# Optimization experiments

Measured on AMD Instinct MI355X. Metric: run time of the kernel, lower is better.

## Reference

```python
import jax, jax.numpy as jnp
import numpy as np

D = 1024      # input_dim
H = 16        # head_num
HD = 64       # head_dim
HID = 4096    # mlp hidden
CUR = 512     # cur_seq
PREV = 512    # prev_seq (memory)
FULL = CUR + PREV
BS = 16
SCALE = 1.0 / (HD ** 0.5)


def setup_inputs() -> dict:
    key = jax.random.key(0)
    ks = jax.random.split(key, 20)
    def nrm(k, shape, s=0.02):
        return (jax.random.normal(k, shape) * s).astype(jnp.float32)
    inp = {
        "inputs": nrm(ks[0], (CUR, BS, D), 1.0),
        "pos_embedding": nrm(ks[1], (FULL, 1, D), 1.0),
        "u": nrm(ks[2], (H, HD)),
        "v": nrm(ks[3], (H, HD)),
        "memory": nrm(ks[4], (PREV, BS, D), 1.0),
        # causal mask: position i (query) may attend to j <= i + PREV; True = masked
        "mask": jnp.triu(jnp.ones((CUR, FULL), dtype=bool), k=PREV + 1)[:, :, None],
        # attention params (stored as (in, out); torch Linear applies x @ W.T + b)
        "Wkv": nrm(ks[5], (D, 2 * H * HD)), "bkv": jnp.zeros((2 * H * HD,), jnp.float32),
        "Wq": nrm(ks[6], (D, H * HD)), "bq": jnp.zeros((H * HD,), jnp.float32),
        "Wo": nrm(ks[7], (H * HD, D)), "bo": jnp.zeros((D,), jnp.float32),
        "Wp": nrm(ks[8], (D, H * HD)), "bp": jnp.zeros((H * HD,), jnp.float32),
        # layernorms
        "ln1_g": jnp.ones((D,), jnp.float32), "ln1_b": jnp.zeros((D,), jnp.float32),
        "ln2_g": jnp.ones((D,), jnp.float32), "ln2_b": jnp.zeros((D,), jnp.float32),
        # mlp (mlp_num=2): Linear(D,HID)+relu, Linear(HID,D)+relu
        "W1": nrm(ks[9], (D, HID)), "b1": jnp.zeros((HID,), jnp.float32),
        "W2": nrm(ks[10], (HID, D)), "b2": jnp.zeros((D,), jnp.float32),
        # GRU gates: stacked [Wr,Wz,Wg] and [Ur,Uz,Ug], no bias; bg init 2.0
        "g1_W": nrm(ks[11], (3, D, D)), "g1_U": nrm(ks[12], (3, D, D)),
        "g1_bg": jnp.full((D,), 2.0, jnp.float32),
        "g2_W": nrm(ks[13], (3, D, D)), "g2_U": nrm(ks[14], (3, D, D)),
        "g2_bg": jnp.full((D,), 2.0, jnp.float32),
    }
    return inp


def _layernorm(x, g, b, eps=1e-5):
    mu = jnp.mean(x, axis=-1, keepdims=True)
    var = jnp.mean(jnp.square(x - mu), axis=-1, keepdims=True)
    return (x - mu) * jax.lax.rsqrt(var + eps) * g + b


def _rel_shift(x):
    # x: (bs, head, cur, full) -> pad/reshape/slice trick of Transformer-XL
    b, h, c, f = x.shape
    xp = jnp.pad(x, ((0, 0), (0, 0), (0, 0), (1, 0)))      # (b,h,c,f+1)
    xp = xp.reshape(b, h, f + 1, c)
    return xp[:, :, 1:, :].reshape(b, h, c, f)


def _gru_gate(x, y, W, U, bg):
    # W, U: (3, D, D) for [r, z, g] gates; torch Linear => y @ W[i].T
    r = jax.nn.sigmoid(y @ W[0].T + x @ U[0].T)
    z = jax.nn.sigmoid(y @ W[1].T + x @ U[1].T - bg)
    h = jnp.tanh(y @ W[2].T + (r * x) @ U[2].T)
    return (1.0 - z) * x + z * h


def _attention_xl(x_cur, pos_emb, x_full, u, v, mask,
                  Wkv, bkv, Wq, bq, Wo, bo, Wp, bp):
    cur, bs, _ = x_cur.shape
    full = x_full.shape[0]
    kv = x_full @ Wkv + bkv                                  # (full, bs, 2*H*HD)
    key, value = jnp.split(kv, 2, axis=-1)
    query = x_cur @ Wq + bq                                  # (cur, bs, H*HD)
    r = (pos_emb @ Wp + bp).reshape(full, H, HD)             # (full, H, HD)

    key = key.reshape(full, bs, H, HD)
    value = value.reshape(full, bs, H, HD)
    query = query.reshape(cur, bs, H, HD)

    content = jnp.einsum('ibhd,jbhd->bhij', query + u, key)  # (bs,H,cur,full)
    position = jnp.einsum('ibhd,jhd->bhij', query + v, r)    # (bs,H,cur,full)
    position = _rel_shift(position)

    attn = (content + position) * SCALE
    # mask: (cur, full, 1) bool, True = masked
    m = mask[:, :, 0][None, None]                            # (1,1,cur,full)
    attn = jnp.where(m, -jnp.inf, attn)
    p = jax.nn.softmax(attn, axis=-1)

    out = jnp.einsum('bhij,jbhd->ibhd', p, value).reshape(cur, bs, H * HD)
    return out @ Wo + bo                                     # (cur, bs, D)


def reference(inputs, pos_embedding, u, v, memory, mask,
              Wkv, bkv, Wq, bq, Wo, bo, Wp, bp,
              ln1_g, ln1_b, ln2_g, ln2_b,
              W1, b1, W2, b2,
              g1_W, g1_U, g1_bg, g2_W, g2_U, g2_bg):
    prev = memory.shape[0]
    full_input = jnp.concatenate([memory, inputs], axis=0)   # (full, bs, D)
    x1 = _layernorm(full_input, ln1_g, ln1_b)
    a1 = _attention_xl(x1[prev:], pos_embedding, x1, u, v, mask,
                       Wkv, bkv, Wq, bq, Wo, bo, Wp, bp)
    a1 = jax.nn.relu(a1)                                     # dropout = identity (eval)
    o1 = _gru_gate(inputs, a1, g1_W, g1_U, g1_bg)
    x2 = _layernorm(o1, ln2_g, ln2_b)
    m2 = jax.nn.relu(jax.nn.relu(x2 @ W1 + b1) @ W2 + b2)    # mlp: act after every linear
    o2 = _gru_gate(o1, m2, g2_W, g2_U, g2_bg)
    return o2
```

## Files before the change

kernel.cpp:

```cpp
#include <hip/hip_runtime.h>
#include <stdint.h>

typedef _Float16 h16;
typedef __attribute__((ext_vector_type(8))) _Float16 f16x8;
typedef __attribute__((ext_vector_type(4))) _Float16 f16x4;
typedef __attribute__((ext_vector_type(4))) float f32x4;

enum { F_OBF = 1, F_BIAS = 2, F_RELU = 4, F_ACC = 8, F_DUAL = 16 };

#define BARRIER_MEM                                  \
  do {                                               \
    asm volatile("" ::: "memory");                   \
    __builtin_amdgcn_s_barrier();                    \
    asm volatile("" ::: "memory");                   \
  } while (0)

static __device__ __forceinline__ void gload16(const void* g, void* l) {
  __builtin_amdgcn_global_load_lds((__attribute__((address_space(1))) void*)g,
                                   (__attribute__((address_space(3))) void*)l,
                                   16, 0, 0);
}

template <int BN, int FLAGS>
__global__ __launch_bounds__(512) void gemm2_k(
    const h16* __restrict__ A, const h16* __restrict__ B,
    void* __restrict__ Cv, const float* __restrict__ bias,
    int K, int lda, int ldb, int ldc, int gm,
    void* __restrict__ C2v, const float* __restrict__ bias2) {
  constexpr int NH = BN / 128;
  constexpr int WN = BN / 4;
  __shared__ h16 Al[2][256][64];
  __shared__ h16 Bl[2][BN][64];

  const int tid = threadIdx.x, lane = tid & 63, wid = tid >> 6;
  const int wr = wid >> 2, wn = wid & 3;
  const int ar = lane & 15, q4 = lane >> 4;

  const int nwg = gridDim.x, cpx = nwg >> 3;
  const int bid = (blockIdx.x & 7) * cpx + (blockIdx.x >> 3);
  const int mx = bid % gm, ny = bid / gm;

  const h16* Ab = A + (long)mx * 256 * lda;
  const h16* Bb = B + (long)ny * BN * ldb;

  auto stageA = [&](int buf, int half, int k0) {
#pragma unroll
    for (int l = 0; l < 2; ++l) {
      const int idx = l * 512 + tid;
      const int row = half * 128 + (idx >> 3), sl = idx & 7;
      gload16(Ab + (long)row * lda + k0 + (sl ^ (row & 7)) * 8,
              (char*)&Al[buf][0][0] + (half * 1024 + l * 512 + wid * 64) * 16);
    }
  };
  auto stageB = [&](int buf, int half, int k0) {
#pragma unroll
    for (int l = 0; l < NH; ++l) {
      const int idx = l * 512 + tid;
      const int row = half * (BN / 2) + (idx >> 3), sl = idx & 7;
      gload16(Bb + (long)row * ldb + k0 + (sl ^ (row & 7)) * 8,
              (char*)&Bl[buf][0][0] + (half * (BN * 4) + l * 512 + wid * 64) * 16);
    }
  };

  f32x4 acc[8][2 * NH] = {};
  const int nk = K >> 6;

  stageB(0, 0, 0); stageB(0, 1, 0); stageA(0, 0, 0); stageA(0, 1, 0);
  if (nk > 1) { stageB(1, 0, 64); stageB(1, 1, 64); stageA(1, 0, 64); stageA(1, 1, 64); }
  if (nk > 1) {
    if constexpr (NH == 2) asm volatile("s_waitcnt vmcnt(8)" ::: "memory");
    else                   asm volatile("s_waitcnt vmcnt(6)" ::: "memory");
  } else {
    asm volatile("s_waitcnt vmcnt(0)" ::: "memory");
  }
  BARRIER_MEM;

  for (int kt = 0; kt < nk; ++kt) {
    const int b = kt & 1;
    const int k2 = (kt + 2) << 6;
    const bool pf = (kt + 2) < nk;

    f16x8 a0[4][2], b0[NH][2];
#pragma unroll
    for (int m = 0; m < 4; ++m) {
      const int row = wr * 128 + m * 16 + ar;
#pragma unroll
      for (int ks = 0; ks < 2; ++ks)
        a0[m][ks] = *(const f16x8*)&Al[b][row][((ks * 4 + q4) ^ (row & 7)) * 8];
    }
#pragma unroll
    for (int n = 0; n < NH; ++n) {
      const int row = wn * WN + n * 16 + ar;
#pragma unroll
      for (int ks = 0; ks < 2; ++ks)
        b0[n][ks] = *(const f16x8*)&Bl[b][row][((ks * 4 + q4) ^ (row & 7)) * 8];
    }
    BARRIER_MEM;
    __builtin_amdgcn_s_setprio(1);
#pragma unroll
    for (int m = 0; m < 4; ++m)
#pragma unroll
      for (int n = 0; n < NH; ++n)
#pragma unroll
        for (int ks = 0; ks < 2; ++ks)
          acc[m][n] = __builtin_amdgcn_mfma_f32_16x16x32_f16(a0[m][ks], b0[n][ks], acc[m][n], 0, 0, 0);
    __builtin_amdgcn_s_setprio(0);
    BARRIER_MEM;

    f16x8 b1f[NH][2];
#pragma unroll
    for (int n = 0; n < NH; ++n) {
      const int row = wn * WN + (n + NH) * 16 + ar;
#pragma unroll
      for (int ks = 0; ks < 2; ++ks)
        b1f[n][ks] = *(const f16x8*)&Bl[b][row][((ks * 4 + q4) ^ (row & 7)) * 8];
    }
    BARRIER_MEM;
    __builtin_amdgcn_s_setprio(1);
#pragma unroll
    for (int m = 0; m < 4; ++m)
#pragma unroll
      for (int n = 0; n < NH; ++n)
#pragma unroll
        for (int ks = 0; ks < 2; ++ks)
          acc[m][n + NH] = __builtin_amdgcn_mfma_f32_16x16x32_f16(a0[m][ks], b1f[n][ks], acc[m][n + NH], 0, 0, 0);
    __builtin_amdgcn_s_setprio(0);
    BARRIER_MEM;

    f16x8 a1f[4][2];
#pragma unroll
    for (int m = 0; m < 4; ++m) {
      const int row = wr * 128 + (m + 4) * 16 + ar;
#pragma unroll
      for (int ks = 0; ks < 2; ++ks)
        a1f[m][ks] = *(const f16x8*)&Al[b][row][((ks * 4 + q4) ^ (row & 7)) * 8];
    }
    if (pf) { stageB(b, 0, k2); stageB(b, 1, k2); }
    BARRIER_MEM;
    __builtin_amdgcn_s_setprio(1);
#pragma unroll
    for (int m = 0; m < 4; ++m)
#pragma unroll
      for (int n = 0; n < NH; ++n)
#pragma unroll
        for (int ks = 0; ks < 2; ++ks)
          acc[m + 4][n] = __builtin_amdgcn_mfma_f32_16x16x32_f16(a1f[m][ks], b0[n][ks], acc[m + 4][n], 0, 0, 0);
    __builtin_amdgcn_s_setprio(0);
    BARRIER_MEM;

    if (pf) { stageA(b, 0, k2); stageA(b, 1, k2); }
    __builtin_amdgcn_s_setprio(1);
#pragma unroll
    for (int m = 0; m < 4; ++m)
#pragma unroll
      for (int n = 0; n < NH; ++n)
#pragma unroll
        for (int ks = 0; ks < 2; ++ks)
          acc[m + 4][n + NH] = __builtin_amdgcn_mfma_f32_16x16x32_f16(a1f[m][ks], b1f[n][ks], acc[m + 4][n + NH], 0, 0, 0);
    __builtin_amdgcn_s_setprio(0);
    if (pf) {
      if constexpr (NH == 2) asm volatile("s_waitcnt vmcnt(8)" ::: "memory");
      else                   asm volatile("s_waitcnt vmcnt(6)" ::: "memory");
    } else if (kt + 1 < nk) {
      asm volatile("s_waitcnt vmcnt(0)" ::: "memory");
    }
    BARRIER_MEM;
  }

#pragma unroll
  for (int m = 0; m < 8; ++m) {
#pragma unroll
    for (int n = 0; n < 2 * NH; ++n) {
      const int col = ny * BN + wn * WN + n * 16 + ar;
      float bv1 = 0.f, bv2 = 0.f;
      if (FLAGS & F_BIAS) bv1 = bias[col];
      if (FLAGS & F_DUAL) bv2 = bias2[col];
#pragma unroll
      for (int r = 0; r < 4; ++r) {
        const int row = mx * 256 + wr * 128 + m * 16 + q4 * 4 + r;
        float val = acc[m][n][r] + bv1;
        if (FLAGS & F_RELU) val = fmaxf(val, 0.f);
        if constexpr ((FLAGS & F_ACC) != 0) {
          float* p = (float*)Cv + (long)row * ldc + col;
          *p = *p + val;
        } else if constexpr ((FLAGS & F_OBF) != 0) {
          ((h16*)Cv)[(long)row * ldc + col] = (h16)val;
          if constexpr ((FLAGS & F_DUAL) != 0)
            ((h16*)C2v)[(long)row * ldc + col] = (h16)(acc[m][n][r] + bv2);
        } else {
          ((float*)Cv)[(long)row * ldc + col] = val;
        }
      }
    }
  }
}

__global__ __launch_bounds__(256) void fattn_k(
    const h16* __restrict__ qu, const h16* __restrict__ qv,
    const h16* __restrict__ kvb, const h16* __restrict__ vT,
    const h16* __restrict__ rb, h16* __restrict__ attn) {
  __shared__ h16 Kl[2][128][64];
  __shared__ h16 Vl[64][128];
  __shared__ h16 Psc[4][16][164];

  const int tid = threadIdx.x, lane = tid & 63, wv = tid >> 6;
  const int z = blockIdx.x, b = z >> 4, h = z & 15;
  const int i0 = blockIdx.y * 64;
  const int ar = lane & 15, q4 = lane >> 4;
  const int myrow = i0 + wv * 16;
  const h16* vTz = vT + (long)z * 64 * 1024;

  const long qoff = ((long)(myrow + ar) * 16 + b) * 1024 + h * 64 + q4 * 8;
  f16x8 quf[2], qvf[2];
  quf[0] = *(const f16x8*)&qu[qoff];
  quf[1] = *(const f16x8*)&qu[qoff + 32];
  qvf[0] = *(const f16x8*)&qv[qoff];
  qvf[1] = *(const f16x8*)&qv[qoff + 32];

  f32x4 o[4] = {};
  float mrow[4], lrow[4];
#pragma unroll
  for (int r = 0; r < 4; ++r) { mrow[r] = -3e38f; lrow[r] = 0.f; }

  const int ntiles = (i0 + 575 + 128) >> 7;

  auto stageK = [&](int buf, int j0) {
#pragma unroll
    for (int it = 0; it < 4; ++it) {
      const int ch = it * 256 + wv * 64 + lane;
      const int kr = ch >> 3, ks = ch & 7;
      gload16(kvb + ((long)(j0 + kr) * 16 + b) * 2048 + h * 64 + (ks ^ (kr & 7)) * 8,
              (char*)&Kl[buf][0][0] + (it * 256 + wv * 64) * 16);
    }
  };
  auto stageV = [&](int j0) {
#pragma unroll
    for (int it = 0; it < 4; ++it) {
      const int ch = it * 256 + wv * 64 + lane;
      const int vd = ch >> 4, vs = ch & 15;
      gload16(vTz + (long)vd * 1024 + j0 + (vs ^ (vd & 7)) * 8,
              (char*)&Vl[0][0] + (it * 256 + wv * 64) * 16);
    }
  };

  stageK(0, 0);
  asm volatile("s_waitcnt vmcnt(0)" ::: "memory");
  __builtin_amdgcn_s_barrier();

  for (int t = 0; t < ntiles; ++t) {
    const int j0 = t * 128;
    const int kb = t & 1;
    const bool pk = (t + 1) < ntiles;

    stageV(j0);
    if (pk) stageK(kb ^ 1, (t + 1) * 128);
    if (pk) asm volatile("s_waitcnt vmcnt(8)" ::: "memory");
    else    asm volatile("s_waitcnt vmcnt(4)" ::: "memory");
    BARRIER_MEM;

    f32x4 acc_c[8] = {};
#pragma unroll
    for (int kd = 0; kd < 2; ++kd)
#pragma unroll
      for (int nf = 0; nf < 8; ++nf) {
        const int j = nf * 16 + ar;
        const int phys = (kd * 4 + q4) ^ (j & 7);
        const f16x8 kf = *(const f16x8*)&Kl[kb][j][phys * 8];
        acc_c[nf] = __builtin_amdgcn_mfma_f32_16x16x32_f16(quf[kd], kf, acc_c[nf], 0, 0, 0);
      }

    const int jbase = j0 - myrow + 496;
    f32x4 acc_p[9] = {};
#pragma unroll
    for (int kd = 0; kd < 2; ++kd)
#pragma unroll
      for (int jf = 0; jf < 9; ++jf) {
        int jjr = jbase + jf * 16 + ar;
        if (jjr > 1023) jjr = 1023;
        const f16x8 rf = *(const f16x8*)&rb[(long)jjr * 1024 + h * 64 + kd * 32 + q4 * 8];
        acc_p[jf] = __builtin_amdgcn_mfma_f32_16x16x32_f16(qvf[kd], rf, acc_p[jf], 0, 0, 0);
      }
#pragma unroll
    for (int jf = 0; jf < 9; ++jf)
#pragma unroll
      for (int r = 0; r < 4; ++r)
        Psc[wv][q4 * 4 + r][jf * 16 + ar] = (h16)acc_p[jf][r];

    float p[8][4];
#pragma unroll
    for (int nf = 0; nf < 8; ++nf)
#pragma unroll
      for (int r = 0; r < 4; ++r) {
        const int iloc = q4 * 4 + r;
        const int jloc = nf * 16 + ar;
        const int band = jloc - iloc + 15;
        const float pv = (float)Psc[wv][iloc][band];
        float sv = (acc_c[nf][r] + pv) * 0.125f;
        const bool ok = (j0 + jloc) <= (myrow + iloc + 512);
        p[nf][r] = ok ? sv : -3e38f;
      }
#pragma unroll
    for (int r = 0; r < 4; ++r) {
      float tm = -3e38f;
#pragma unroll
      for (int nf = 0; nf < 8; ++nf) tm = fmaxf(tm, p[nf][r]);
      tm = fmaxf(tm, __shfl_xor(tm, 1));
      tm = fmaxf(tm, __shfl_xor(tm, 2));
      tm = fmaxf(tm, __shfl_xor(tm, 4));
      tm = fmaxf(tm, __shfl_xor(tm, 8));
      const float mn = fmaxf(mrow[r], tm);
      const float sc = __expf(mrow[r] - mn);
      mrow[r] = mn;
      float ts = 0.f;
#pragma unroll
      for (int nf = 0; nf < 8; ++nf) {
        const float e = __expf(p[nf][r] - mn);
        p[nf][r] = e;
        ts += e;
      }
      ts += __shfl_xor(ts, 1);
      ts += __shfl_xor(ts, 2);
      ts += __shfl_xor(ts, 4);
      ts += __shfl_xor(ts, 8);
      lrow[r] = lrow[r] * sc + ts;
#pragma unroll
      for (int v = 0; v < 4; ++v) o[v][r] *= sc;
    }

#pragma unroll
    for (int nf = 0; nf < 8; ++nf)
#pragma unroll
      for (int r = 0; r < 4; ++r) {
        const int iloc = q4 * 4 + r, jloc = nf * 16 + ar;
        Psc[wv][iloc][((jloc >> 3) ^ (iloc & 7)) * 8 + (jloc & 7)] = (h16)p[nf][r];
      }

    if (pk) asm volatile("s_waitcnt vmcnt(4)" ::: "memory");
    else    asm volatile("s_waitcnt vmcnt(0)" ::: "memory");
    BARRIER_MEM;

#pragma unroll
    for (int ks = 0; ks < 4; ++ks) {
      const f16x8 pa = *(const f16x8*)&Psc[wv][ar][((ks * 4 + q4) ^ (ar & 7)) * 8];
#pragma unroll
      for (int vnf = 0; vnf < 4; ++vnf) {
        const int d = vnf * 16 + ar;
        const f16x8 vb = *(const f16x8*)&Vl[d][((ks * 4 + q4) ^ (d & 7)) * 8];
        o[vnf] = __builtin_amdgcn_mfma_f32_16x16x32_f16(pa, vb, o[vnf], 0, 0, 0);
      }
    }
    BARRIER_MEM;
  }

#pragma unroll
  for (int vnf = 0; vnf < 4; ++vnf)
#pragma unroll
    for (int r = 0; r < 4; ++r) {
      const int i_ = myrow + q4 * 4 + r;
      attn[((long)i_ * 16 + b) * 1024 + h * 64 + vnf * 16 + ar] =
          (h16)(o[vnf][r] / lrow[r]);
    }
}

__global__ __launch_bounds__(256) void wtrans_k(const float* __restrict__ in,
                                                h16* __restrict__ out, int K, int N) {
  __shared__ float t[32][33];
  const int tx = threadIdx.x & 31, ty = threadIdx.x >> 5;
  const int n0 = blockIdx.x * 32, k0 = blockIdx.y * 32;
#pragma unroll
  for (int j = 0; j < 32; j += 8)
    t[ty + j][tx] = in[(long)(k0 + ty + j) * N + n0 + tx];
  __syncthreads();
#pragma unroll
  for (int j = 0; j < 32; j += 8)
    out[(long)(n0 + ty + j) * K + k0 + tx] = (h16)t[tx][ty + j];
}

__global__ __launch_bounds__(256) void cast_k(const float* __restrict__ in,
                                              h16* __restrict__ out, long n4) {
  const long i = (long)blockIdx.x * 256 + threadIdx.x;
  if (i >= n4) return;
  const float4 v = ((const float4*)in)[i];
  f16x4 o;
  o[0] = (h16)v.x; o[1] = (h16)v.y; o[2] = (h16)v.z; o[3] = (h16)v.w;
  ((f16x4*)out)[i] = o;
}

__global__ __launch_bounds__(256) void gateprep_k(
    const float* __restrict__ W1g, const float* __restrict__ U1g,
    const float* __restrict__ W2g, const float* __restrict__ U2g,
    h16* __restrict__ o1, h16* __restrict__ o2) {
  const long i = (long)blockIdx.x * 256 + threadIdx.x;
  const long elem = i * 4;
  const int row = (int)(elem >> 11);
  const int col = (int)(elem & 2047);
  const int gate = row >> 10, oc = row & 1023;
  const float* W = (blockIdx.y == 0) ? W1g : W2g;
  const float* U = (blockIdx.y == 0) ? U1g : U2g;
  h16* out = (blockIdx.y == 0) ? o1 : o2;
  const float* src = (col < 1024)
      ? (W + (long)gate * 1048576 + (long)oc * 1024 + col)
      : (U + (long)gate * 1048576 + (long)oc * 1024 + (col - 1024));
  const float4 v = *(const float4*)src;
  f16x4 o;
  o[0] = (h16)v.x; o[1] = (h16)v.y; o[2] = (h16)v.z; o[3] = (h16)v.w;
  *(f16x4*)(out + elem) = o;
}

__global__ __launch_bounds__(256) void xcast_k(const float* __restrict__ in,
                                               h16* __restrict__ yx) {
  const long i = (long)blockIdx.x * 256 + threadIdx.x;
  const long row = i >> 8;
  const int c4 = (int)(i & 255);
  const float4 v = ((const float4*)in)[i];
  f16x4 o;
  o[0] = (h16)v.x; o[1] = (h16)v.y; o[2] = (h16)v.z; o[3] = (h16)v.w;
  *(f16x4*)(yx + row * 2048 + 1024 + c4 * 4) = o;
}

__global__ void addbias_k(const float* __restrict__ bq, const float* __restrict__ u,
                          const float* __restrict__ v, float* __restrict__ qu,
                          float* __restrict__ qv) {
  const int c = blockIdx.x * 256 + threadIdx.x;
  if (c < 1024) { qu[c] = bq[c] + u[c]; qv[c] = bq[c] + v[c]; }
}

__global__ __launch_bounds__(256) void zero_out_k(float* __restrict__ out, long n) {
  const long i = (long)blockIdx.x * 256 + threadIdx.x;
  if (i < n) out[i] = 0.f;
}

__global__ __launch_bounds__(256) void ln_k(const float* __restrict__ src0,
                                            const float* __restrict__ src1, int rows0,
                                            const float* __restrict__ g,
                                            const float* __restrict__ b,
                                            h16* __restrict__ out) {
  const int row = blockIdx.x, tid = threadIdx.x;
  const float* src = (row < rows0) ? (src0 + (long)row * 1024)
                                   : (src1 + (long)(row - rows0) * 1024);
  const float4 x = ((const float4*)src)[tid];
  float s = x.x + x.y + x.z + x.w;
  float sq = x.x * x.x + x.y * x.y + x.z * x.z + x.w * x.w;
#pragma unroll
  for (int o = 32; o > 0; o >>= 1) { s += __shfl_down(s, o); sq += __shfl_down(sq, o); }
  __shared__ float red[8];
  const int lane = tid & 63, w = tid >> 6;
  if (lane == 0) { red[w] = s; red[4 + w] = sq; }
  __syncthreads();
  s = red[0] + red[1] + red[2] + red[3];
  sq = red[4] + red[5] + red[6] + red[7];
  const float mu = s * (1.f / 1024.f);
  const float inv = rsqrtf(sq * (1.f / 1024.f) - mu * mu + 1e-5f);
  const float4 gg = ((const float4*)g)[tid], bb = ((const float4*)b)[tid];
  f16x4 o;
  o[0] = (h16)((x.x - mu) * inv * gg.x + bb.x);
  o[1] = (h16)((x.y - mu) * inv * gg.y + bb.y);
  o[2] = (h16)((x.z - mu) * inv * gg.z + bb.z);
  o[3] = (h16)((x.w - mu) * inv * gg.w + bb.w);
  ((f16x4*)(out + (long)row * 1024))[tid] = o;
}

__global__ __launch_bounds__(256) void vtrans_k(const h16* __restrict__ kv,
                                                h16* __restrict__ vT) {
  const int z = blockIdx.y, b = z >> 4, h = z & 15;
  const int j0 = blockIdx.x * 64;
  __shared__ h16 t[64][72];
  const int jj = threadIdx.x >> 3, c = threadIdx.x & 7;
#pragma unroll
  for (int half = 0; half < 2; ++half) {
    const int j = jj + half * 32;
    const f16x8 v = *(const f16x8*)(kv + ((long)(j0 + j) * 16 + b) * 2048 + 1024 + h * 64 + c * 8);
    *(f16x8*)&t[j][c * 8] = v;
  }
  __syncthreads();
#pragma unroll
  for (int half = 0; half < 2; ++half) {
    const int d = jj + half * 32;
    f16x8 o;
#pragma unroll
    for (int k = 0; k < 8; ++k) o[k] = t[c * 8 + k][d];
    *(f16x8*)(vT + ((long)z * 64 + d) * 1024 + j0 + c * 8) = o;
  }
}

__global__ __launch_bounds__(256) void gru_rx_k(const float* __restrict__ T,
                                                const float* __restrict__ x,
                                                h16* __restrict__ yx) {
  const long i = (long)blockIdx.x * 256 + threadIdx.x;
  const long row = i >> 8;
  const int c4 = (int)(i & 255);
  const float4 t = *((const float4*)(T + row * 2048) + c4);
  const float4 xx = ((const float4*)x)[i];
  f16x4 o;
  o[0] = (h16)(xx.x / (1.f + __expf(-t.x)));
  o[1] = (h16)(xx.y / (1.f + __expf(-t.y)));
  o[2] = (h16)(xx.z / (1.f + __expf(-t.z)));
  o[3] = (h16)(xx.w / (1.f + __expf(-t.w)));
  *(f16x4*)(yx + row * 2048 + 1024 + c4 * 4) = o;
}

__global__ __launch_bounds__(256) void gru_out_k(const float* __restrict__ T,
                                                 const float* __restrict__ G,
                                                 const float* __restrict__ x,
                                                 const float* __restrict__ bg,
                                                 float* __restrict__ outf,
                                                 h16* __restrict__ outh) {
  const long i = (long)blockIdx.x * 256 + threadIdx.x;
  const long row = i >> 8;
  const int c4 = (int)(i & 255);
  const float4 tz = *((const float4*)(T + row * 2048 + 1024) + c4);
  const float4 th = *((const float4*)(G + row * 1024) + c4);
  const float4 xx = ((const float4*)x)[i];
  const float4 bb = ((const float4*)bg)[c4];
  float4 o;
  {
    const float z0 = 1.f / (1.f + __expf(-(tz.x - bb.x)));
    const float z1 = 1.f / (1.f + __expf(-(tz.y - bb.y)));
    const float z2 = 1.f / (1.f + __expf(-(tz.z - bb.z)));
    const float z3 = 1.f / (1.f + __expf(-(tz.w - bb.w)));
    o.x = (1.f - z0) * xx.x + z0 * tanhf(th.x);
    o.y = (1.f - z1) * xx.y + z1 * tanhf(th.y);
    o.z = (1.f - z2) * xx.z + z2 * tanhf(th.z);
    o.w = (1.f - z3) * xx.w + z3 * tanhf(th.w);
  }
  ((float4*)outf)[i] = o;
  if (outh != nullptr) {
    f16x4 oh;
    oh[0] = (h16)o.x; oh[1] = (h16)o.y; oh[2] = (h16)o.z; oh[3] = (h16)o.w;
    *(f16x4*)(outh + row * 2048 + 1024 + c4 * 4) = oh;
  }
}

extern "C" void kernel_launch(void* const* d_in, const int* in_sizes, int n_in,
                              void* d_out, int out_size, void* d_ws, size_t ws_size,
                              hipStream_t stream) {
  const float* inputs = (const float*)d_in[0];
  const float* pos    = (const float*)d_in[1];
  const float* u      = (const float*)d_in[2];
  const float* v      = (const float*)d_in[3];
  const float* memory = (const float*)d_in[4];
  const float* Wkv = (const float*)d_in[6];  const float* bkv = (const float*)d_in[7];
  const float* Wq  = (const float*)d_in[8];  const float* bq  = (const float*)d_in[9];
  const float* Wo  = (const float*)d_in[10]; const float* bo  = (const float*)d_in[11];
  const float* Wp  = (const float*)d_in[12]; const float* bp  = (const float*)d_in[13];
  const float* ln1_g = (const float*)d_in[14]; const float* ln1_b = (const float*)d_in[15];
  const float* ln2_g = (const float*)d_in[16]; const float* ln2_b = (const float*)d_in[17];
  const float* W1 = (const float*)d_in[18]; const float* b1 = (const float*)d_in[19];
  const float* W2 = (const float*)d_in[20]; const float* b2 = (const float*)d_in[21];
  const float* g1_W = (const float*)d_in[22]; const float* g1_U = (const float*)d_in[23];
  const float* g1_bg = (const float*)d_in[24];
  const float* g2_W = (const float*)d_in[25]; const float* g2_U = (const float*)d_in[26];
  const float* g2_bg = (const float*)d_in[27];
  (void)in_sizes; (void)n_in;

  const size_t MB = 1u << 20;
  const size_t NEEDED = 247 * MB;
  const dim3 blk(256);
  if (ws_size < NEEDED) {
    zero_out_k<<<(out_size + 255) / 256, blk, 0, stream>>>((float*)d_out, out_size);
    return;
  }

  char* w = (char*)d_ws;
  h16* WoT   = (h16*)(w + 0 * MB);
  h16* W1T   = (h16*)(w + 2 * MB);
  h16* W2T   = (h16*)(w + 10 * MB);
  h16* g1B   = (h16*)(w + 18 * MB);
  h16* g2B   = (h16*)(w + 30 * MB);
  h16* WkvT  = (h16*)(w + 42 * MB);
  h16* WqT   = (h16*)(w + 46 * MB);
  h16* WpT   = (h16*)(w + 48 * MB);
  h16* posb  = (h16*)(w + 50 * MB);
  float* bias_qu = (float*)(w + 52 * MB);
  float* bias_qv = (float*)(w + 52 * MB + 8192);
  h16* yx1   = (h16*)(w + 53 * MB);
  h16* x1    = (h16*)(w + 85 * MB);
  char* Rbig =        w + 117 * MB;
  h16* qu    = (h16*)(w + 181 * MB);
  h16* qv    = (h16*)(w + 197 * MB);
  h16* attn  = (h16*)(w + 213 * MB);
  h16* rb    = (h16*)(w + 245 * MB);

  h16*   kvb  = (h16*)Rbig;
  float* Trz  = (float*)Rbig;
  h16*   h1   = (h16*)Rbig;
  float* Tg   = (float*)qu;
  h16*   vT   = x1;
  h16*   yx2  = x1;
  float* o1f  = (float*)attn;
  h16*   x2   = yx1;

  wtrans_k<<<dim3(64, 32), blk, 0, stream>>>(Wkv, WkvT, 1024, 2048);
  wtrans_k<<<dim3(32, 32), blk, 0, stream>>>(Wq, WqT, 1024, 1024);
  wtrans_k<<<dim3(32, 32), blk, 0, stream>>>(Wo, WoT, 1024, 1024);
  wtrans_k<<<dim3(32, 32), blk, 0, stream>>>(Wp, WpT, 1024, 1024);
  wtrans_k<<<dim3(128, 32), blk, 0, stream>>>(W1, W1T, 1024, 4096);
  wtrans_k<<<dim3(32, 128), blk, 0, stream>>>(W2, W2T, 4096, 1024);
  gateprep_k<<<dim3(6144, 2), blk, 0, stream>>>(g1_W, g1_U, g2_W, g2_U, g1B, g2B);
  cast_k<<<1024, blk, 0, stream>>>(pos, posb, 262144);
  xcast_k<<<8192, blk, 0, stream>>>(inputs, yx1);
  addbias_k<<<4, blk, 0, stream>>>(bq, u, v, bias_qu, bias_qv);

  ln_k<<<16384, blk, 0, stream>>>(memory, inputs, 8192, ln1_g, ln1_b, x1);

  gemm2_k<256, F_OBF | F_BIAS><<<dim3(512), dim3(512), 0, stream>>>(
      x1, WkvT, kvb, bkv, 1024, 1024, 1024, 2048, 64, nullptr, nullptr);
  gemm2_k<128, F_OBF | F_BIAS | F_DUAL><<<dim3(256), dim3(512), 0, stream>>>(
      x1 + 8192L * 1024, WqT, qu, bias_qu, 1024, 1024, 1024, 1024, 32, qv, bias_qv);
  gemm2_k<128, F_OBF | F_BIAS><<<dim3(32), dim3(512), 0, stream>>>(
      posb, WpT, rb, bp, 1024, 1024, 1024, 1024, 4, nullptr, nullptr);
  vtrans_k<<<dim3(16, 256), blk, 0, stream>>>(kvb, vT);

  fattn_k<<<dim3(256, 8), blk, 0, stream>>>(qu, qv, kvb, vT, rb, attn);

  gemm2_k<128, F_OBF | F_BIAS | F_RELU><<<dim3(256), dim3(512), 0, stream>>>(
      attn, WoT, yx1, bo, 1024, 1024, 1024, 2048, 32, nullptr, nullptr);

  gemm2_k<256, 0><<<dim3(256), dim3(512), 0, stream>>>(
      yx1, g1B, Trz, nullptr, 2048, 2048, 2048, 2048, 32, nullptr, nullptr);
  gru_rx_k<<<8192, blk, 0, stream>>>(Trz, inputs, yx1);
  gemm2_k<128, 0><<<dim3(256), dim3(512), 0, stream>>>(
      yx1, g1B + 2048L * 2048, Tg, nullptr, 2048, 2048, 2048, 1024, 32, nullptr, nullptr);
  gru_out_k<<<8192, blk, 0, stream>>>(Trz, Tg, inputs, g1_bg, o1f, yx2);

  ln_k<<<8192, blk, 0, stream>>>(o1f, o1f, 8192, ln2_g, ln2_b, x2);
  gemm2_k<256, F_OBF | F_BIAS | F_RELU><<<dim3(512), dim3(512), 0, stream>>>(
      x2, W1T, h1, b1, 1024, 1024, 1024, 4096, 32, nullptr, nullptr);
  gemm2_k<128, F_OBF | F_BIAS | F_RELU><<<dim3(256), dim3(512), 0, stream>>>(
      h1, W2T, yx2, b2, 4096, 4096, 4096, 2048, 32, nullptr, nullptr);

  gemm2_k<256, 0><<<dim3(256), dim3(512), 0, stream>>>(
      yx2, g2B, Trz, nullptr, 2048, 2048, 2048, 2048, 32, nullptr, nullptr);
  gru_rx_k<<<8192, blk, 0, stream>>>(Trz, o1f, yx2);
  gemm2_k<128, 0><<<dim3(256), dim3(512), 0, stream>>>(
      yx2, g2B + 2048L * 2048, Tg, nullptr, 2048, 2048, 2048, 1024, 32, nullptr, nullptr);
  gru_out_k<<<8192, blk, 0, stream>>>(Trz, Tg, o1f, g2_bg, (float*)d_out, nullptr);
}
```

Measured before the change: 1.007 ms.

## Fuse GRU gate elementwise ops into GEMM epilogues with double-buffered inputs

Removes the separate gru_rx and gru_out elementwise kernels by computing the reset-gate sigmoid*x and the final GRU blend inside the GEMM epilogues. The z-gate preactivation is now stored in fp16 instead of fp32, and the Wo and W2 GEMMs write their output twice (dual buffers), so the r*x product can be written into a separate buffer while the first GEMM is still reading the original. This saves kernel launches and the fp32 round trips of the gate intermediates. In exchange the epilogues do more scattered scalar loads and stores, and storing z in fp16 adds precision loss.

```diff
diff --git a/kernel.cpp b/kernel.cpp
--- a/kernel.cpp
+++ b/kernel.cpp
@@ -6,7 +6,7 @@
 typedef __attribute__((ext_vector_type(4))) _Float16 f16x4;
 typedef __attribute__((ext_vector_type(4))) float f32x4;
 
-enum { F_OBF = 1, F_BIAS = 2, F_RELU = 4, F_ACC = 8, F_DUAL = 16 };
+enum { F_OBF = 1, F_BIAS = 2, F_RELU = 4, F_ACC = 8, F_DUAL = 16, F_GRX = 32, F_GOUT = 64 };
 
 #define BARRIER_MEM                                  \
   do {                                               \
@@ -26,7 +26,9 @@
     const h16* __restrict__ A, const h16* __restrict__ B,
     void* __restrict__ Cv, const float* __restrict__ bias,
     int K, int lda, int ldb, int ldc, int gm,
-    void* __restrict__ C2v, const float* __restrict__ bias2) {
+    void* __restrict__ C2v, const float* __restrict__ bias2,
+    const float* __restrict__ xf, const float* __restrict__ bgp,
+    const h16* __restrict__ tzp) {
   constexpr int NH = BN / 128;
   constexpr int WN = BN / 4;
   __shared__ h16 Al[2][256][64];
@@ -180,13 +182,32 @@
         const int row = mx * 256 + wr * 128 + m * 16 + q4 * 4 + r;
         float val = acc[m][n][r] + bv1;
         if (FLAGS & F_RELU) val = fmaxf(val, 0.f);
-        if constexpr ((FLAGS & F_ACC) != 0) {
+        if constexpr ((FLAGS & F_GRX) != 0) {
+          if (col < 1024) {
+            const float rr = 1.f / (1.f + __expf(-val));
+            ((h16*)Cv)[(long)row * 2048 + 1024 + col] =
+                (h16)(rr * xf[(long)row * 1024 + col]);
+          } else {
+            ((h16*)C2v)[(long)row * 1024 + col - 1024] = (h16)val;
+          }
+        } else if constexpr ((FLAGS & F_GOUT) != 0) {
+          const float zp = (float)tzp[(long)row * 1024 + col] - bgp[col];
+          const float zz = 1.f / (1.f + __expf(-zp));
+          const float xv = xf[(long)row * 1024 + col];
+          const float oo = (1.f - zz) * xv + zz * tanhf(val);
+          ((float*)Cv)[(long)row * 1024 + col] = oo;
+          if (C2v != nullptr)
+            ((h16*)C2v)[(long)row * 2048 + 1024 + col] = (h16)oo;
+        } else if constexpr ((FLAGS & F_ACC) != 0) {
           float* p = (float*)Cv + (long)row * ldc + col;
           *p = *p + val;
         } else if constexpr ((FLAGS & F_OBF) != 0) {
           ((h16*)Cv)[(long)row * ldc + col] = (h16)val;
-          if constexpr ((FLAGS & F_DUAL) != 0)
-            ((h16*)C2v)[(long)row * ldc + col] = (h16)(acc[m][n][r] + bv2);
+          if constexpr ((FLAGS & F_DUAL) != 0) {
+            float v2 = acc[m][n][r] + bv2;
+            if (FLAGS & F_RELU) v2 = fmaxf(v2, 0.f);
+            ((h16*)C2v)[(long)row * ldc + col] = (h16)v2;
+          }
         } else {
           ((float*)Cv)[(long)row * ldc + col] = val;
         }
@@ -480,54 +501,6 @@
 #pragma unroll
     for (int k = 0; k < 8; ++k) o[k] = t[c * 8 + k][d];
     *(f16x8*)(vT + ((long)z * 64 + d) * 1024 + j0 + c * 8) = o;
-  }
-}
-
-__global__ __launch_bounds__(256) void gru_rx_k(const float* __restrict__ T,
-                                                const float* __restrict__ x,
-                                                h16* __restrict__ yx) {
-  const long i = (long)blockIdx.x * 256 + threadIdx.x;
-  const long row = i >> 8;
-  const int c4 = (int)(i & 255);
-  const float4 t = *((const float4*)(T + row * 2048) + c4);
-  const float4 xx = ((const float4*)x)[i];
-  f16x4 o;
-  o[0] = (h16)(xx.x / (1.f + __expf(-t.x)));
-  o[1] = (h16)(xx.y / (1.f + __expf(-t.y)));
-  o[2] = (h16)(xx.z / (1.f + __expf(-t.z)));
-  o[3] = (h16)(xx.w / (1.f + __expf(-t.w)));
-  *(f16x4*)(yx + row * 2048 + 1024 + c4 * 4) = o;
-}
-
-__global__ __launch_bounds__(256) void gru_out_k(const float* __restrict__ T,
-                                                 const float* __restrict__ G,
-                                                 const float* __restrict__ x,
-                                                 const float* __restrict__ bg,
-                                                 float* __restrict__ outf,
-                                                 h16* __restrict__ outh) {
-  const long i = (long)blockIdx.x * 256 + threadIdx.x;
-  const long row = i >> 8;
-  const int c4 = (int)(i & 255);
-  const float4 tz = *((const float4*)(T + row * 2048 + 1024) + c4);
-  const float4 th = *((const float4*)(G + row * 1024) + c4);
-  const float4 xx = ((const float4*)x)[i];
-  const float4 bb = ((const float4*)bg)[c4];
-  float4 o;
-  {
-    const float z0 = 1.f / (1.f + __expf(-(tz.x - bb.x)));
-    const float z1 = 1.f / (1.f + __expf(-(tz.y - bb.y)));
-    const float z2 = 1.f / (1.f + __expf(-(tz.z - bb.z)));
-    const float z3 = 1.f / (1.f + __expf(-(tz.w - bb.w)));
-    o.x = (1.f - z0) * xx.x + z0 * tanhf(th.x);
-    o.y = (1.f - z1) * xx.y + z1 * tanhf(th.y);
-    o.z = (1.f - z2) * xx.z + z2 * tanhf(th.z);
-    o.w = (1.f - z3) * xx.w + z3 * tanhf(th.w);
-  }
-  ((float4*)outf)[i] = o;
-  if (outh != nullptr) {
-    f16x4 oh;
-    oh[0] = (h16)o.x; oh[1] = (h16)o.y; oh[2] = (h16)o.z; oh[3] = (h16)o.w;
-    *(f16x4*)(outh + row * 2048 + 1024 + c4 * 4) = oh;
   }
 }
 
@@ -573,7 +546,7 @@
   h16* posb  = (h16*)(w + 50 * MB);
   float* bias_qu = (float*)(w + 52 * MB);
   float* bias_qv = (float*)(w + 52 * MB + 8192);
-  h16* yx1   = (h16*)(w + 53 * MB);
+  h16* yx1A  = (h16*)(w + 53 * MB);
   h16* x1    = (h16*)(w + 85 * MB);
   char* Rbig =        w + 117 * MB;
   h16* qu    = (h16*)(w + 181 * MB);
@@ -582,13 +555,14 @@
   h16* rb    = (h16*)(w + 245 * MB);
 
   h16*   kvb  = (h16*)Rbig;
-  float* Trz  = (float*)Rbig;
+  h16*   Tz   = (h16*)Rbig;
   h16*   h1   = (h16*)Rbig;
-  float* Tg   = (float*)qu;
   h16*   vT   = x1;
-  h16*   yx2  = x1;
+  h16*   yx1B = x1;
+  h16*   x2   = x1;
+  h16*   yx2A = qu;
+  h16*   yx2B = yx1A;
   float* o1f  = (float*)attn;
-  h16*   x2   = yx1;
 
   wtrans_k<<<dim3(64, 32), blk, 0, stream>>>(Wkv, WkvT, 1024, 2048);
   wtrans_k<<<dim3(32, 32), blk, 0, stream>>>(Wq, WqT, 1024, 1024);
@@ -598,41 +572,47 @@
   wtrans_k<<<dim3(32, 128), blk, 0, stream>>>(W2, W2T, 4096, 1024);
   gateprep_k<<<dim3(6144, 2), blk, 0, stream>>>(g1_W, g1_U, g2_W, g2_U, g1B, g2B);
   cast_k<<<1024, blk, 0, stream>>>(pos, posb, 262144);
-  xcast_k<<<8192, blk, 0, stream>>>(inputs, yx1);
+  xcast_k<<<8192, blk, 0, stream>>>(inputs, yx1A);
   addbias_k<<<4, blk, 0, stream>>>(bq, u, v, bias_qu, bias_qv);
 
   ln_k<<<16384, blk, 0, stream>>>(memory, inputs, 8192, ln1_g, ln1_b, x1);
 
   gemm2_k<256, F_OBF | F_BIAS><<<dim3(512), dim3(512), 0, stream>>>(
-      x1, WkvT, kvb, bkv, 1024, 1024, 1024, 2048, 64, nullptr, nullptr);
+      x1, WkvT, kvb, bkv, 1024, 1024, 1024, 2048, 64, nullptr, nullptr,
+      nullptr, nullptr, nullptr);
   gemm2_k<128, F_OBF | F_BIAS | F_DUAL><<<dim3(256), dim3(512), 0, stream>>>(
-      x1 + 8192L * 1024, WqT, qu, bias_qu, 1024, 1024, 1024, 1024, 32, qv, bias_qv);
+      x1 + 8192L * 1024, WqT, qu, bias_qu, 1024, 1024, 1024, 1024, 32, qv, bias_qv,
+      nullptr, nullptr, nullptr);
   gemm2_k<128, F_OBF | F_BIAS><<<dim3(32), dim3(512), 0, stream>>>(
-      posb, WpT, rb, bp, 1024, 1024, 1024, 1024, 4, nullptr, nullptr);
+      posb, WpT, rb, bp, 1024, 1024, 1024, 1024, 4, nullptr, nullptr,
+      nullptr, nullptr, nullptr);
   vtrans_k<<<dim3(16, 256), blk, 0, stream>>>(kvb, vT);
 
   fattn_k<<<dim3(256, 8), blk, 0, stream>>>(qu, qv, kvb, vT, rb, attn);
 
-  gemm2_k<128, F_OBF | F_BIAS | F_RELU><<<dim3(256), dim3(512), 0, stream>>>(
-      attn, WoT, yx1, bo, 1024, 1024, 1024, 2048, 32, nullptr, nullptr);
-
-  gemm2_k<256, 0><<<dim3(256), dim3(512), 0, stream>>>(
-      yx1, g1B, Trz, nullptr, 2048, 2048, 2048, 2048, 32, nullptr, nullptr);
-  gru_rx_k<<<8192, blk, 0, stream>>>(Trz, inputs, yx1);
-  gemm2_k<128, 0><<<dim3(256), dim3(512), 0, stream>>>(
-      yx1, g1B + 2048L * 2048, Tg, nullptr, 2048, 2048, 2048, 1024, 32, nullptr, nullptr);
-  gru_out_k<<<8192, blk, 0, stream>>>(Trz, Tg, inputs, g1_bg, o1f, yx2);
+  gemm2_k<128, F_OBF | F_BIAS | F_RELU | F_DUAL><<<dim3(256), dim3(512), 0, stream>>>(
+      attn, WoT, yx1A, bo, 1024, 1024, 1024, 2048, 32, yx1B, bo,
+      nullptr, nullptr, nullptr);
+
+  gemm2_k<256, F_GRX><<<dim3(256), dim3(512), 0, stream>>>(
+      yx1A, g1B, yx1B, nullptr, 2048, 2048, 2048, 2048, 32, Tz, nullptr,
+      inputs, nullptr, nullptr);
+  gemm2_k<128, F_GOUT><<<dim3(256), dim3(512), 0, stream>>>(
+      yx1B, g1B + 2048L * 2048, o1f, nullptr, 2048, 2048, 2048, 1024, 32, yx2A, nullptr,
+      inputs, g1_bg, Tz);
 
   ln_k<<<8192, blk, 0, stream>>>(o1f, o1f, 8192, ln2_g, ln2_b, x2);
   gemm2_k<256, F_OBF | F_BIAS | F_RELU><<<dim3(512), dim3(512), 0, stream>>>(
-      x2, W1T, h1, b1, 1024, 1024, 1024, 4096, 32, nullptr, nullptr);
-  gemm2_k<128, F_OBF | F_BIAS | F_RELU><<<dim3(256), dim3(512), 0, stream>>>(
-      h1, W2T, yx2, b2, 4096, 4096, 4096, 2048, 32, nullptr, nullptr);
-
-  gemm2_k<256, 0><<<dim3(256), dim3(512), 0, stream>>>(
-      yx2, g2B, Trz, nullptr, 2048, 2048, 2048, 2048, 32, nullptr, nullptr);
-  gru_rx_k<<<8192, blk, 0, stream>>>(Trz, o1f, yx2);
-  gemm2_k<128, 0><<<dim3(256), dim3(512), 0, stream>>>(
-      yx2, g2B + 2048L * 2048, Tg, nullptr, 2048, 2048, 2048, 1024, 32, nullptr, nullptr);
-  gru_out_k<<<8192, blk, 0, stream>>>(Trz, Tg, o1f, g2_bg, (float*)d_out, nullptr);
-}
+      x2, W1T, h1, b1, 1024, 1024, 1024, 4096, 32, nullptr, nullptr,
+      nullptr, nullptr, nullptr);
+  gemm2_k<128, F_OBF | F_BIAS | F_RELU | F_DUAL><<<dim3(256), dim3(512), 0, stream>>>(
+      h1, W2T, yx2A, b2, 4096, 4096, 4096, 2048, 32, yx2B, b2,
+      nullptr, nullptr, nullptr);
+
+  gemm2_k<256, F_GRX><<<dim3(256), dim3(512), 0, stream>>>(
+      yx2A, g2B, yx2B, nullptr, 2048, 2048, 2048, 2048, 32, Tz, nullptr,
+      o1f, nullptr, nullptr);
+  gemm2_k<128, F_GOUT><<<dim3(256), dim3(512), 0, stream>>>(
+      yx2B, g2B + 2048L * 2048, d_out, nullptr, 2048, 2048, 2048, 1024, 32,
+      nullptr, nullptr, o1f, g2_bg, Tz);
+}
```

Measured after the change: 1.054 ms. 1.05x slower.
